# Kernel optimization log

Measured on AMD Instinct MI355X. Metric: run time of the kernel, lower is better.

## Reference

```python
import jax, jax.numpy as jnp
import numpy as np

S_DIM = 4096
N_NODES = 4096
N_EDGES = 32768


def _coarsen(ei_np, N):
    """Integer-only greedy coarsening, faithful to MNGRAPH.forward's while-loop.
    Returns (select order, flattened neighbor indices, segment ids, per-hub
    neighbor counts, forward-fill indices replicating the stale-M behavior for
    empty neighborhoods, and the remapped final edge_index)."""
    ei = ei_np.astype(np.int64).copy()
    I = np.bincount(ei[0], minlength=N)
    O = np.bincount(ei[1], minlength=N)
    order = np.argsort(-(I + O), kind='stable')  # torch.argsort(D, descending=True)
    visits = np.zeros(N, dtype=bool)
    select = []
    nbr_idx, nbr_seg, counts = [], [], []
    while order.size > 0:
        node = int(order[0])
        select.append(node)
        visits[node] = True
        # H = unique neighbors of node in the CURRENT (rewritten) edge_index
        H = np.unique(np.concatenate([ei[1][ei[0] == node], ei[0][ei[1] == node]]))
        visits[H] = True
        order = order[~visits[order]]
        # rewrite: endpoints in H that are not already-selected hubs -> node
        Hn = H[~np.isin(H, np.asarray(select, dtype=np.int64))]
        ei[np.isin(ei, Hn)] = node
        ei = ei[:, ei[0] != ei[1]]  # drop self-loops
        # append reversed edges that are not already present (pair-code isin
        # == the original O(E^2) all/any comparison, computed efficiently)
        code = ei[0] * N + ei[1]
        rcode = ei[1] * N + ei[0]
        new = ~np.isin(rcode, code)
        ei = np.concatenate([ei, ei[::-1][:, new]], axis=1)
        k = len(select) - 1
        nbr_idx.append(H)
        nbr_seg.append(np.full(H.shape[0], k, dtype=np.int64))
        counts.append(H.shape[0])
    select = np.asarray(select, dtype=np.int64)
    sort_sel = np.sort(select)
    ei_out = np.searchsorted(sort_sel, ei)  # compact node ids
    counts = np.asarray(counts, dtype=np.int64)
    # forward-fill: when H is empty the original appends the previous (stale) M
    fill = np.arange(select.shape[0])
    for i in range(select.shape[0]):
        if counts[i] == 0:
            fill[i] = fill[i - 1] if i > 0 else 0
    nbr = np.concatenate(nbr_idx) if nbr_idx else np.zeros(0, np.int64)
    seg = np.concatenate(nbr_seg) if nbr_seg else np.zeros(0, np.int64)
    return select, nbr, seg, counts, fill, ei_out


def setup_inputs() -> dict:
    key = jax.random.key(0)
    k1, k2, k3, k4 = jax.random.split(key, 4)
    x = jax.random.normal(k1, (N_NODES, S_DIM), dtype=jnp.float32)
    edge_index = jax.random.randint(k2, (2, N_EDGES), 0, N_NODES, dtype=jnp.int64)
    bound = float(np.sqrt(6.0 / (1.0 + S_DIM)))  # xavier_uniform on (1, S)
    W1 = jax.random.uniform(k3, (S_DIM,), jnp.float32, -bound, bound)
    W2 = jax.random.uniform(k4, (S_DIM,), jnp.float32, -bound, bound)
    B1 = jnp.zeros((S_DIM,), jnp.float32)
    B2 = jnp.zeros((S_DIM,), jnp.float32)
    return {"x": x, "edge_index": edge_index, "W1": W1, "W2": W2, "B1": B1, "B2": B2}


def reference(x, edge_index, W1, W2, B1, B2):
    N = x.shape[0]
    sel, nbr, seg, counts, fill, ei_out = _coarsen(np.asarray(edge_index), N)
    K = sel.shape[0]
    # Dn = x[n]*W1+B1 for every neighbor of every hub; per-hub mean via segment_sum
    Dn = x[jnp.asarray(nbr)] * W1 + B1                      # [T, S]
    sums = jax.ops.segment_sum(Dn, jnp.asarray(seg), num_segments=K)
    denom = jnp.maximum(jnp.asarray(counts), 1).astype(x.dtype)[:, None]
    mean_Dn = sums / denom                                  # [K, S]
    Dv = x[jnp.asarray(sel)] * W2 + B2                      # [K, S]
    END = jnp.concatenate([Dv, mean_Dn], axis=1)            # [K, 2S]
    END = END[jnp.asarray(fill)]                            # stale-M replication
    return END, jnp.asarray(ei_out)
```

## Files before the change

### kernel.cpp

```cpp
#include <hip/hip_runtime.h>
#include <hip/hip_bf16.h>

#define NT 1024
#define NNODES 4096
#define ECAP 65536

__global__ __launch_bounds__(256)
void zeroBM(int4* __restrict__ bm) {
    bm[(size_t)blockIdx.x * 256 + threadIdx.x] = make_int4(0, 0, 0, 0);
}

__device__ __forceinline__ int blockScanExcl(int v, int* s_w, int* total) {
    const int tid  = threadIdx.x;
    const int lane = tid & 63;
    const int wv   = tid >> 6;
    int x = v;
#pragma unroll
    for (int off = 1; off < 64; off <<= 1) {
        int t = __shfl_up(x, off, 64);
        if (lane >= off) x += t;
    }
    if (lane == 63) s_w[wv] = x;
    __syncthreads();
    if (tid < 16) {
        int y = s_w[tid];
#pragma unroll
        for (int off = 1; off < 16; off <<= 1) {
            int t = __shfl_up(y, off, 16);
            if (tid >= off) y += t;
        }
        s_w[tid] = y;
    }
    __syncthreads();
    int base = wv ? s_w[wv - 1] : 0;
    int tot  = s_w[15];
    __syncthreads();
    *total = tot;
    return base + x - v;
}

__global__ __launch_bounds__(NT, 1)
void phaseA1(const int* __restrict__ ei, int E0,
             int* __restrict__ U, int* __restrict__ V,
             unsigned int* __restrict__ BM,
             int* __restrict__ NBR, int* __restrict__ OTH,
             int* __restrict__ ORDV, int* __restrict__ ROFFG, int* __restrict__ RENDG,
             int* __restrict__ HAND)
{
    __shared__ unsigned short s_order[NNODES];
    __shared__ unsigned char  s_vis[NNODES];
    __shared__ unsigned char  s_rank[NNODES];
    __shared__ unsigned int   s_hb[NNODES / 32];
    __shared__ int s_roff[NNODES];
    __shared__ int s_rend[NNODES];
    __shared__ int s_tmp[NNODES];
    __shared__ int s_mat[64][65];
    __shared__ int s_w[16];
    __shared__ int s_bc[16];

    const int tid = threadIdx.x;

    for (int i = tid; i < NNODES; i += NT) { s_vis[i] = 0; s_tmp[i] = 0; }
    for (int i = tid; i < NNODES / 32; i += NT) s_hb[i] = 0;
    if (tid < 16) s_bc[tid] = 0;
    __syncthreads();

    for (int i = tid; i < E0; i += NT)
        if (ei[2 * i + 1] != 0) s_bc[9] = 1;
    __syncthreads();
    const int is64 = !s_bc[9];

    for (int e = tid; e < E0; e += NT) {
        int uu = ei[is64 ? 2 * e : e];
        int vv = ei[is64 ? 2 * (E0 + e) : (E0 + e)];
        U[e] = uu; V[e] = vv;
        atomicAdd(&s_tmp[uu], 1);
        atomicAdd(&s_tmp[vv], 1);
    }
    __syncthreads();
    for (int n = tid; n < NNODES; n += NT) atomicMax(&s_bc[7], s_tmp[n]);
    __syncthreads();
    const int maxd = s_bc[7];

    if (maxd < 64) {
        const int wv = tid >> 6, lane = tid & 63;
        const unsigned long long ltm = (1ull << lane) - 1ull;
        for (int g = wv; g < 64; g += 16) {
            int n = g * 64 + lane;
            int d = s_tmp[n];
            int rk = 0;
            for (int dd = 0; dd < 64; ++dd) {
                unsigned long long bal = __ballot(d == dd);
                if (lane == 0) s_mat[dd][g] = __popcll(bal);
                if (d == dd) rk = __popcll(bal & ltm);
            }
            s_rank[n] = (unsigned char)rk;
        }
        __syncthreads();
        if (tid < 64) {
            int run = 0;
            for (int g = 0; g < 64; ++g) { int t = s_mat[tid][g]; s_mat[tid][g] = run; run += t; }
            s_mat[tid][64] = run;
        }
        __syncthreads();
        if (tid < 64) {
            int x = s_mat[tid][64];
#pragma unroll
            for (int off = 1; off < 64; off <<= 1) {
                int t = __shfl_up(x, off, 64);
                if (tid >= off) x += t;
            }
            int T = __shfl(x, 63, 64);
            s_mat[tid][64] = T - x;
        }
        __syncthreads();
        for (int g = wv; g < 64; g += 16) {
            int n = g * 64 + lane;
            int d = s_tmp[n];
            int pos = s_mat[d][64] + s_mat[d][g] + (int)s_rank[n];
            s_order[pos] = (unsigned short)n;
        }
        __syncthreads();
    } else {
        for (int d = maxd; d >= 0; --d) {
            int n0 = tid * 4;
            int f0 = (s_tmp[n0] == d), f1 = (s_tmp[n0 + 1] == d);
            int f2 = (s_tmp[n0 + 2] == d), f3 = (s_tmp[n0 + 3] == d);
            int tot;
            int off = blockScanExcl(f0 + f1 + f2 + f3, s_w, &tot);
            int idx = s_bc[4] + off;
            if (f0) s_order[idx++] = (unsigned short)n0;
            if (f1) s_order[idx++] = (unsigned short)(n0 + 1);
            if (f2) s_order[idx++] = (unsigned short)(n0 + 2);
            if (f3) s_order[idx++] = (unsigned short)(n0 + 3);
            __syncthreads();
            if (tid == 0) s_bc[4] += tot;
            __syncthreads();
        }
    }

    if (tid == 0) {
        int nd = s_order[0];
        s_bc[0] = nd; s_vis[nd] = 1;
    }
    __syncthreads();
    {
        const int node = s_bc[0];
        for (int e = tid; e < E0; e += NT) {
            int uu = U[e], vv = V[e];
            if (uu == node) {
                int w = vv; unsigned m = 1u << (w & 31);
                unsigned old = atomicOr(&s_hb[w >> 5], m);
                if (!(old & m)) { int i = atomicAdd(&s_bc[2], 1); s_tmp[i] = w; s_vis[w] = 1; }
            }
            if (vv == node) {
                int w = uu; unsigned m = 1u << (w & 31);
                unsigned old = atomicOr(&s_hb[w >> 5], m);
                if (!(old & m)) { int i = atomicAdd(&s_bc[2], 1); s_tmp[i] = w; s_vis[w] = 1; }
            }
        }
        __syncthreads();
        for (int e = tid; e < E0; e += NT) {
            int uu = U[e];
            if (uu != node && ((s_hb[uu >> 5] >> (uu & 31)) & 1)) U[e] = node;
            int vv = V[e];
            if (vv != node && ((s_hb[vv >> 5] >> (vv & 31)) & 1)) V[e] = node;
        }
        __syncthreads();
    }

    for (int e = tid; e < E0; e += NT) {
        int uu = U[e], vv = V[e];
        if (uu != vv) {
            unsigned code = ((unsigned)uu << 12) | (unsigned)vv;
            atomicOr(&BM[code >> 5], 1u << (code & 31));
        }
    }
    __syncthreads();
    for (int t0 = 0; t0 < E0; t0 += NT * 32) {
        unsigned fm = 0u;
        const int base = t0 + tid * 32;
        for (int j = 0; j < 32; ++j) {
            int e = base + j;
            if (e < E0) {
                int uu = U[e], vv = V[e];
                if (uu != vv) {
                    unsigned rc = ((unsigned)vv << 12) | (unsigned)uu;
                    unsigned old = atomicOr(&BM[rc >> 5], 0u);
                    if (!((old >> (rc & 31)) & 1u)) fm |= (1u << j);
                }
            }
        }
        int tot;
        int off = blockScanExcl(__popc(fm), s_w, &tot);
        int r = s_bc[5] + off;
        unsigned m = fm;
        while (m) {
            int j = __ffs((int)m) - 1; m &= m - 1;
            int e = base + j;
            U[E0 + r] = V[e]; V[E0 + r] = U[e];
            ++r;
        }
        __syncthreads();
        if (tid == 0) s_bc[5] += tot;
        __syncthreads();
    }
    const int E1 = E0 + s_bc[5];

    for (int n = tid; n < NNODES; n += NT) s_roff[n] = 0;
    __syncthreads();
    for (int e = tid; e < E1; e += NT) {
        int uu = U[e], vv = V[e];
        if (uu != vv) atomicAdd(&s_roff[uu], 1);
    }
    __syncthreads();
    {
        int n0 = tid * 4;
        int c0 = s_roff[n0], c1 = s_roff[n0 + 1], c2 = s_roff[n0 + 2], c3 = s_roff[n0 + 3];
        int tot;
        int off = blockScanExcl(c0 + c1 + c2 + c3, s_w, &tot);
        int st = off;
        s_roff[n0] = st;     s_rend[n0] = st;     st += c0;
        s_roff[n0 + 1] = st; s_rend[n0 + 1] = st; st += c1;
        s_roff[n0 + 2] = st; s_rend[n0 + 2] = st; st += c2;
        s_roff[n0 + 3] = st; s_rend[n0 + 3] = st;
    }
    __syncthreads();
    for (int e = tid; e < E1; e += NT) {
        int uu = U[e], vv = V[e];
        if (uu != vv) {
            int p = atomicAdd(&s_rend[uu], 1);
            OTH[p] = vv;
        }
    }
    __syncthreads();
    {
        const int cnt0 = s_bc[2];
        for (int i = tid; i < cnt0; i += NT) NBR[i] = s_tmp[i];
    }
    for (int i = tid; i < NNODES; i += NT) {
        int nd = (int)s_order[i];
        ORDV[i]  = nd | (s_vis[nd] ? 0x8000 : 0);
        ROFFG[i] = s_roff[i];
        RENDG[i] = s_rend[i];
    }
    if (tid == 0) { HAND[0] = E1; HAND[1] = s_bc[2]; HAND[2] = s_bc[0]; }
}

__global__ __launch_bounds__(64, 1)
void phaseA2(const int* __restrict__ OTH, int* __restrict__ NBR,
             const int* __restrict__ ORDV, const int* __restrict__ ROFFG,
             const int* __restrict__ RENDG, const int* __restrict__ HAND,
             int* __restrict__ SEL, int* __restrict__ CNTS,
             int* __restrict__ NST, int* __restrict__ FIL, int* __restrict__ SC,
             int* __restrict__ LABG, int* __restrict__ RNKG)
{
    __shared__ unsigned short s_ordvis[NNODES];
    __shared__ unsigned short s_pos[NNODES];
    __shared__ unsigned short s_lab[NNODES];
    __shared__ unsigned short s_so[NNODES];
    __shared__ int s_cnt[NNODES];
    __shared__ int s_stamp[NNODES];
    __shared__ int s_roff[NNODES];
    __shared__ int s_rend[NNODES];
    __shared__ unsigned char s_sel[NNODES];

    const int ln = threadIdx.x;
    const unsigned long long ltm = (1ull << ln) - 1ull;
    const int cnt0 = HAND[1], hub0 = HAND[2];

    for (int i = ln; i < NNODES; i += 64) {
        int ov = ORDV[i];
        s_ordvis[i] = (unsigned short)ov;
        s_pos[ov & 0x7FFF] = (unsigned short)i;
        s_roff[i] = ROFFG[i];
        s_rend[i] = RENDG[i];
        s_lab[i] = (unsigned short)i;
        s_stamp[i] = 0; s_sel[i] = 0; s_cnt[i] = 0;
    }
    if (ln == 0) {
        s_sel[hub0] = 1; s_so[0] = (unsigned short)hub0;
        s_cnt[0] = cnt0;
    }

    int nc = cnt0;
    int p = 0, k = 1;
    int pf_node = -1, pf_rb = 0, pf_re = 0, pf_val = -1;

    for (;;) {
        int node = -1;
        while (p < NNODES) {
            int idx = p + ln;
            int ov = (idx < NNODES) ? (int)s_ordvis[idx] : 0x8000;
            unsigned long long bal = __ballot(!(ov & 0x8000));
            if (bal != 0ull) {
                int sl = __ffsll((long long)bal) - 1;
                node = __shfl(ov, sl, 64) & 0x7FFF;
                p += sl + 1;
                break;
            }
            p += 64;
        }
        if (node < 0) break;
        if (ln == 0) { s_sel[node] = 1; s_so[k] = (unsigned short)node; }

        int rb, re, v0;
        if (node == pf_node) { rb = pf_rb; re = pf_re; v0 = pf_val; }
        else {
            rb = s_roff[node]; re = s_rend[node];
            v0 = (rb + ln < re) ? OTH[rb + ln] : -1;
        }

        {
            int q = p, cand = -1, cidx = NNODES;
            while (q < NNODES) {
                int idx = q + ln;
                int ov = (idx < NNODES) ? (int)s_ordvis[idx] : 0x8000;
                unsigned long long bal = __ballot(!(ov & 0x8000));
                if (bal != 0ull) {
                    int sl = __ffsll((long long)bal) - 1;
                    cand = __shfl(ov, sl, 64) & 0x7FFF;
                    cidx = q + sl;
                    break;
                }
                q += 64;
            }
            p = (cand >= 0) ? cidx : NNODES;
            pf_node = cand;
            if (cand >= 0) {
                pf_rb = s_roff[cand]; pf_re = s_rend[cand];
                pf_val = (pf_rb + ln < pf_re) ? OTH[pf_rb + ln] : -1;
            } else pf_val = -1;
        }

        const int begin = nc;
        auto proc = [&](int o) {
            int w = (o >= 0) ? (int)s_lab[o] : node;
            bool cnd = (w != node);
            int old = k;
            if (cnd) old = atomicMax(&s_stamp[w], k);
            bool nw = cnd && (old < k);
            unsigned long long bal = __ballot(nw);
            if (nw) {
                int pre = __popcll(bal & ltm);
                NBR[nc + pre] = w;
                s_ordvis[s_pos[w]] = (unsigned short)(0x8000 | w);
                if (!s_sel[w]) s_lab[w] = (unsigned short)node;
            }
            nc += __popcll(bal);
        };
        proc(v0);
        for (int s0 = rb + 64; s0 < re; s0 += 64) {
            int o = (s0 + ln < re) ? OTH[s0 + ln] : -1;
            proc(o);
        }
        if (ln == 0) s_cnt[k] = nc - begin;
        k++;
    }
    const int K = k;

    {
        int base = 0;
        for (int c = 0; c < NNODES / 64; ++c) {
            int n = c * 64 + ln;
            int f = s_sel[n];
            unsigned long long b = __ballot(f);
            s_stamp[n] = base + __popcll(b & ltm);
            base += __popcll(b);
        }
    }
    {
        int nb = 0;
        for (int c = 0; c * 64 < K; ++c) {
            int i = c * 64 + ln;
            int cv = (i < K) ? s_cnt[i] : 0;
            int x = cv;
#pragma unroll
            for (int off = 1; off < 64; off <<= 1) {
                int t = __shfl_up(x, off, 64);
                if (ln >= off) x += t;
            }
            if (i < K) { NST[i] = nb + x - cv; CNTS[i] = cv; SEL[i] = (int)s_so[i]; }
            nb += __shfl(x, 63, 64);
        }
    }
    {
        int carry = 0;
        for (int c = 0; c * 64 < K; ++c) {
            int i = c * 64 + ln;
            int f = (i < K) && (s_cnt[i] > 0);
            unsigned long long b = __ballot(f);
            unsigned long long m = b & ((ln == 63) ? ~0ull : ((1ull << (ln + 1)) - 1ull));
            int fil = m ? (c * 64 + 63 - __clzll(m)) : carry;
            if (i < K) FIL[i] = fil;
            carry = b ? (c * 64 + 63 - __clzll(b)) : carry;
        }
    }
    if (ln == 0) SC[0] = K;
    for (int i = ln; i < NNODES; i += 64) {
        LABG[i] = (int)s_lab[i];
        RNKG[i] = s_stamp[i];
    }
}

__global__ __launch_bounds__(NT, 1)
void phaseA3(const int* __restrict__ U, const int* __restrict__ V,
             const int* __restrict__ LABG, const int* __restrict__ RNKG,
             const int* __restrict__ HAND, int* __restrict__ SC,
             int* __restrict__ TMP, float* __restrict__ out)
{
    __shared__ unsigned short l_lab[NNODES];
    __shared__ int l_rnk[NNODES];
    __shared__ int s_w[16];
    __shared__ int s_base[1];

    const int tid = threadIdx.x;
    for (int i = tid; i < NNODES; i += NT) {
        l_lab[i] = (unsigned short)LABG[i];
        l_rnk[i] = RNKG[i];
    }
    if (tid == 0) s_base[0] = 0;
    __syncthreads();

    const int E1 = HAND[0];
    const int K  = SC[0];
    const size_t obase = (size_t)K * 8192;

    for (int t0 = 0; t0 < E1; t0 += NT * 64) {
        unsigned long long fm = 0ull;
        const int base = t0 + tid * 64;
        if (base + 64 <= E1) {
            const int4* U4 = (const int4*)(U + base);
            const int4* V4 = (const int4*)(V + base);
#pragma unroll
            for (int q = 0; q < 16; ++q) {
                int4 a = U4[q], b = V4[q];
                int j = q * 4;
                if ((int)l_lab[a.x] != (int)l_lab[b.x]) fm |= 1ull << j;
                if ((int)l_lab[a.y] != (int)l_lab[b.y]) fm |= 1ull << (j + 1);
                if ((int)l_lab[a.z] != (int)l_lab[b.z]) fm |= 1ull << (j + 2);
                if ((int)l_lab[a.w] != (int)l_lab[b.w]) fm |= 1ull << (j + 3);
            }
        } else {
            for (int j = 0; j < 64; ++j) {
                int e = base + j;
                if (e < E1) {
                    if ((int)l_lab[U[e]] != (int)l_lab[V[e]]) fm |= 1ull << j;
                }
            }
        }
        int tot;
        int off = blockScanExcl(__popcll(fm), s_w, &tot);
        int r = s_base[0] + off;
        unsigned long long m = fm;
        while (m) {
            int j = __ffsll((long long)m) - 1; m &= m - 1;
            int e = base + j;
            out[obase + (size_t)r] = (float)l_rnk[(int)l_lab[U[e]]];
            TMP[r] = l_rnk[(int)l_lab[V[e]]];
            ++r;
        }
        __syncthreads();
        if (tid == 0) s_base[0] += tot;
        __syncthreads();
    }
    const int Ef = s_base[0];
    if (tid == 0) SC[1] = Ef;
    for (int r = tid; r < Ef; r += NT)
        out[obase + (size_t)Ef + (size_t)r] = (float)TMP[r];
}

__global__ __launch_bounds__(256, 4)
void phaseB(const float* __restrict__ x,
            const float* __restrict__ W1, const float* __restrict__ W2,
            const float* __restrict__ B1, const float* __restrict__ B2,
            const int* __restrict__ NBR, const int* __restrict__ SEL,
            const int* __restrict__ CNTS, const int* __restrict__ NST,
            const int* __restrict__ FIL, const int* __restrict__ SC,
            float* __restrict__ out)
{
    const int K = SC[0];
    const int k = blockIdx.x;
    if (k >= K) return;
    const int kk   = FIL[k];
    const int node = SEL[kk];
    const int cnt  = CNTS[kk];
    const int st   = NST[kk];
    const int tid  = threadIdx.x;
    const float4* x4 = (const float4*)x;

    float4 acc[4];
#pragma unroll
    for (int j = 0; j < 4; j++) acc[j] = make_float4(0.f, 0.f, 0.f, 0.f);

    for (int r = 0; r < cnt; ++r) {
        const float4* row = x4 + (size_t)NBR[st + r] * 1024;
#pragma unroll
        for (int j = 0; j < 4; j++) {
            float4 t = row[tid + j * 256];
            acc[j].x += t.x; acc[j].y += t.y; acc[j].z += t.z; acc[j].w += t.w;
        }
    }

    const float fc  = (float)cnt;
    const float inv = 1.0f / (float)(cnt > 1 ? cnt : 1);
    const float4* xr = x4 + (size_t)node * 1024;
    float4* o4 = (float4*)(out + (size_t)k * 8192);

#pragma unroll
    for (int j = 0; j < 4; j++) {
        int c = tid + j * 256;
        float4 w1 = ((const float4*)W1)[c], b1 = ((const float4*)B1)[c];
        float4 w2 = ((const float4*)W2)[c], b2 = ((const float4*)B2)[c];
        float4 xv = xr[c];
        float4 pd, pm;
        pd.x = xv.x * w2.x + b2.x;
        pd.y = xv.y * w2.y + b2.y;
        pd.z = xv.z * w2.z + b2.z;
        pd.w = xv.w * w2.w + b2.w;
        pm.x = (acc[j].x * w1.x + fc * b1.x) * inv;
        pm.y = (acc[j].y * w1.y + fc * b1.y) * inv;
        pm.z = (acc[j].z * w1.z + fc * b1.z) * inv;
        pm.w = (acc[j].w * w1.w + fc * b1.w) * inv;
        o4[c] = pd;
        o4[1024 + c] = pm;
    }
}

extern "C" void kernel_launch(void* const* d_in, const int* in_sizes, int n_in,
                              void* d_out, int out_size, void* d_ws, size_t ws_size,
                              hipStream_t stream)
{
    const float* x  = (const float*)d_in[0];
    const int*   ei = (const int*)d_in[1];
    const float* W1 = (const float*)d_in[2];
    const float* W2 = (const float*)d_in[3];
    const float* B1 = (const float*)d_in[4];
    const float* B2 = (const float*)d_in[5];
    const int E0 = in_sizes[1] / 2;

    char* w = (char*)d_ws;
    int* U = (int*)w;
    int* V = U + ECAP;
    unsigned int* BM = (unsigned int*)(V + ECAP);
    int* OTH = (int*)BM;
    int* NBR = OTH + 2 * ECAP;
    int* TMP = NBR + 2 * ECAP;
    char* meta = (char*)BM + (2u << 20);
    int* SEL   = (int*)meta;
    int* CNTS  = SEL  + NNODES;
    int* NST   = CNTS + NNODES;
    int* FIL   = NST  + NNODES;
    int* SC    = FIL  + NNODES;
    int* ORDV  = SC   + 16;
    int* ROFFG = ORDV + NNODES;
    int* RENDG = ROFFG + NNODES;
    int* LABG  = RENDG + NNODES;
    int* RNKG  = LABG + NNODES;
    int* HAND  = RNKG + NNODES;
    float* out = (float*)d_out;

    hipLaunchKernelGGL(zeroBM, dim3(512), dim3(256), 0, stream, (int4*)BM);

    hipLaunchKernelGGL(phaseA1, dim3(1), dim3(NT), 0, stream,
                       ei, E0, U, V, BM, NBR, OTH, ORDV, ROFFG, RENDG, HAND);
    hipLaunchKernelGGL(phaseA2, dim3(1), dim3(64), 0, stream,
                       OTH, NBR, ORDV, ROFFG, RENDG, HAND,
                       SEL, CNTS, NST, FIL, SC, LABG, RNKG);
    hipLaunchKernelGGL(phaseA3, dim3(1), dim3(NT), 0, stream,
                       U, V, LABG, RNKG, HAND, SC, TMP, out);
    hipLaunchKernelGGL(phaseB, dim3(NNODES), dim3(256), 0, stream,
                       x, W1, W2, B1, B2, NBR, SEL, CNTS, NST, FIL, SC, out);
}
```

Before: 1.190 ms.

## Replace ordered-visit scan with bitmask and speculatively select two hubs per step

The serial greedy hub-selection loop in phaseA2 now tracks visited order slots as a 4096-bit LDS bitmap instead of flag bits in a ushort array. The next unvisited hub is found with two ballots and find-first-set over 128 words rather than a linear 64-wide scan. Each iteration picks two candidate hubs at once and prefetches both adjacency rows. It re-selects the second hub if processing the first marks it visited. The aim is to shorten the serial critical path of one wavefront, at the cost of extra LDS atomics and more complex control flow.

Measured after the change: 1.061 ms. 10.9% less time.

```diff
diff --git a/kernel.cpp b/kernel.cpp
--- a/kernel.cpp
+++ b/kernel.cpp
@@ -255,7 +255,8 @@
              int* __restrict__ NST, int* __restrict__ FIL, int* __restrict__ SC,
              int* __restrict__ LABG, int* __restrict__ RNKG)
 {
-    __shared__ unsigned short s_ordvis[NNODES];
+    __shared__ unsigned short s_ord[NNODES];
+    __shared__ unsigned int   s_visbits[NNODES / 32];
     __shared__ unsigned short s_pos[NNODES];
     __shared__ unsigned short s_lab[NNODES];
     __shared__ unsigned short s_so[NNODES];
@@ -269,14 +270,17 @@
     const unsigned long long ltm = (1ull << ln) - 1ull;
     const int cnt0 = HAND[1], hub0 = HAND[2];
 
+    for (int i = ln; i < NNODES / 32; i += 64) s_visbits[i] = 0u;
     for (int i = ln; i < NNODES; i += 64) {
         int ov = ORDV[i];
-        s_ordvis[i] = (unsigned short)ov;
-        s_pos[ov & 0x7FFF] = (unsigned short)i;
+        int nd = ov & 0x7FFF;
+        s_ord[i] = (unsigned short)nd;
+        s_pos[nd] = (unsigned short)i;
         s_roff[i] = ROFFG[i];
         s_rend[i] = RENDG[i];
         s_lab[i] = (unsigned short)i;
         s_stamp[i] = 0; s_sel[i] = 0; s_cnt[i] = 0;
+        if (ov & 0x8000) atomicOr(&s_visbits[i >> 5], 1u << (i & 31));
     }
     if (ln == 0) {
         s_sel[hub0] = 1; s_so[0] = (unsigned short)hub0;
@@ -284,59 +288,76 @@
     }
 
     int nc = cnt0;
-    int p = 0, k = 1;
-    int pf_node = -1, pf_rb = 0, pf_re = 0, pf_val = -1;
-
-    for (;;) {
-        int node = -1;
-        while (p < NNODES) {
-            int idx = p + ln;
-            int ov = (idx < NNODES) ? (int)s_ordvis[idx] : 0x8000;
-            unsigned long long bal = __ballot(!(ov & 0x8000));
-            if (bal != 0ull) {
-                int sl = __ffsll((long long)bal) - 1;
-                node = __shfl(ov, sl, 64) & 0x7FFF;
-                p += sl + 1;
-                break;
-            }
-            p += 64;
-        }
-        if (node < 0) break;
-        if (ln == 0) { s_sel[node] = 1; s_so[k] = (unsigned short)node; }
-
-        int rb, re, v0;
-        if (node == pf_node) { rb = pf_rb; re = pf_re; v0 = pf_val; }
-        else {
-            rb = s_roff[node]; re = s_rend[node];
-            v0 = (rb + ln < re) ? OTH[rb + ln] : -1;
-        }
-
-        {
-            int q = p, cand = -1, cidx = NNODES;
-            while (q < NNODES) {
-                int idx = q + ln;
-                int ov = (idx < NNODES) ? (int)s_ordvis[idx] : 0x8000;
-                unsigned long long bal = __ballot(!(ov & 0x8000));
-                if (bal != 0ull) {
-                    int sl = __ffsll((long long)bal) - 1;
-                    cand = __shfl(ov, sl, 64) & 0x7FFF;
-                    cidx = q + sl;
-                    break;
+    int k = 1;
+
+    auto select2 = [&](int& c1, int& c2) {
+        unsigned lo = ~s_visbits[ln];
+        unsigned hi = ~s_visbits[ln + 64];
+        unsigned long long ball = __ballot(lo != 0u);
+        unsigned long long balh = __ballot(hi != 0u);
+        c1 = -1; c2 = -1;
+        int slot2 = -1;
+        if (ball) {
+            int sl = __ffsll((long long)ball) - 1;
+            unsigned ww = __shfl(lo, sl, 64);
+            int slot1 = sl * 32 + __ffs((int)ww) - 1;
+            c1 = (int)s_ord[slot1];
+            unsigned wwb = ww & (ww - 1);
+            if (wwb) slot2 = sl * 32 + __ffs((int)wwb) - 1;
+            else {
+                unsigned long long ball2 = ball & (ball - 1);
+                if (ball2) {
+                    int sl2 = __ffsll((long long)ball2) - 1;
+                    unsigned ww2 = __shfl(lo, sl2, 64);
+                    slot2 = sl2 * 32 + __ffs((int)ww2) - 1;
+                } else if (balh) {
+                    int sl2 = __ffsll((long long)balh) - 1;
+                    unsigned ww2 = __shfl(hi, sl2, 64);
+                    slot2 = 2048 + sl2 * 32 + __ffs((int)ww2) - 1;
                 }
-                q += 64;
-            }
-            p = (cand >= 0) ? cidx : NNODES;
-            pf_node = cand;
-            if (cand >= 0) {
-                pf_rb = s_roff[cand]; pf_re = s_rend[cand];
-                pf_val = (pf_rb + ln < pf_re) ? OTH[pf_rb + ln] : -1;
-            } else pf_val = -1;
-        }
-
-        const int begin = nc;
-        auto proc = [&](int o) {
-            int w = (o >= 0) ? (int)s_lab[o] : node;
-            bool cnd = (w != node);
+            }
+        } else if (balh) {
+            int sl = __ffsll((long long)balh) - 1;
+            unsigned ww = __shfl(hi, sl, 64);
+            int slot1 = 2048 + sl * 32 + __ffs((int)ww) - 1;
+            c1 = (int)s_ord[slot1];
+            unsigned wwb = ww & (ww - 1);
+            if (wwb) slot2 = 2048 + sl * 32 + __ffs((int)wwb) - 1;
+            else {
+                unsigned long long balh2 = balh & (balh - 1);
+                if (balh2) {
+                    int sl2 = __ffsll((long long)balh2) - 1;
+                    unsigned ww2 = __shfl(hi, sl2, 64);
+                    slot2 = 2048 + sl2 * 32 + __ffs((int)ww2) - 1;
+                }
+            }
+        }
+        if (slot2 >= 0) c2 = (int)s_ord[slot2];
+    };
+
+    auto select1 = [&](int& c) {
+        unsigned lo = ~s_visbits[ln];
+        unsigned hi = ~s_visbits[ln + 64];
+        unsigned long long ball = __ballot(lo != 0u);
+        unsigned long long balh = __ballot(hi != 0u);
+        c = -1;
+        if (ball) {
+            int sl = __ffsll((long long)ball) - 1;
+            unsigned ww = __shfl(lo, sl, 64);
+            c = (int)s_ord[sl * 32 + __ffs((int)ww) - 1];
+        } else if (balh) {
+            int sl = __ffsll((long long)balh) - 1;
+            unsigned ww = __shfl(hi, sl, 64);
+            c = (int)s_ord[2048 + sl * 32 + __ffs((int)ww) - 1];
+        }
+    };
+
+    auto procRow = [&](int hub, int rb, int re, int o0, int watch) -> bool {
+        bool invw = false;
+        int o = o0;
+        for (int s0 = rb; s0 < re; s0 += 64) {
+            int w = (o >= 0) ? (int)s_lab[o] : hub;
+            bool cnd = (w != hub);
             int old = k;
             if (cnd) old = atomicMax(&s_stamp[w], k);
             bool nw = cnd && (old < k);
@@ -344,16 +365,59 @@
             if (nw) {
                 int pre = __popcll(bal & ltm);
                 NBR[nc + pre] = w;
-                s_ordvis[s_pos[w]] = (unsigned short)(0x8000 | w);
-                if (!s_sel[w]) s_lab[w] = (unsigned short)node;
+                int slot = (int)s_pos[w];
+                atomicOr(&s_visbits[slot >> 5], 1u << (slot & 31));
+                if (!s_sel[w]) s_lab[w] = (unsigned short)hub;
             }
             nc += __popcll(bal);
-        };
-        proc(v0);
-        for (int s0 = rb + 64; s0 < re; s0 += 64) {
-            int o = (s0 + ln < re) ? OTH[s0 + ln] : -1;
-            proc(o);
-        }
+            invw = invw || (__ballot(nw && (w == watch)) != 0ull);
+            int s1 = s0 + 64;
+            o = (s1 + ln < re) ? OTH[s1 + ln] : -1;
+        }
+        return invw;
+    };
+
+    for (;;) {
+        int c1, c2;
+        select2(c1, c2);
+        if (c1 < 0) break;
+
+        int rb1 = s_roff[c1], re1 = s_rend[c1];
+        int rb2 = (c2 >= 0) ? s_roff[c2] : 0;
+        int re2 = (c2 >= 0) ? s_rend[c2] : 0;
+        int oA = (rb1 + ln < re1) ? OTH[rb1 + ln] : -1;
+        int oB = (c2 >= 0 && rb2 + ln < re2) ? OTH[rb2 + ln] : -1;
+
+        if (ln == 0) {
+            s_sel[c1] = 1; s_so[k] = (unsigned short)c1;
+            int sl1 = (int)s_pos[c1];
+            atomicOr(&s_visbits[sl1 >> 5], 1u << (sl1 & 31));
+            if (c2 >= 0) {
+                int sl2 = (int)s_pos[c2];
+                atomicOr(&s_visbits[sl2 >> 5], 1u << (sl2 & 31));
+            }
+        }
+
+        int begin = nc;
+        bool inval = procRow(c1, rb1, re1, oA, c2);
+        if (ln == 0) s_cnt[k] = nc - begin;
+        k++;
+
+        if (c2 < 0) continue;
+
+        if (inval) {
+            select1(c2);
+            if (c2 < 0) continue;
+            rb2 = s_roff[c2]; re2 = s_rend[c2];
+            oB = (rb2 + ln < re2) ? OTH[rb2 + ln] : -1;
+        }
+        if (ln == 0) {
+            s_sel[c2] = 1; s_so[k] = (unsigned short)c2;
+            int sl2 = (int)s_pos[c2];
+            atomicOr(&s_visbits[sl2 >> 5], 1u << (sl2 & 31));
+        }
+        begin = nc;
+        procRow(c2, rb2, re2, oB, -1);
         if (ln == 0) s_cnt[k] = nc - begin;
         k++;
     }
```

## Use visited bitmask and batch four hub candidates per iteration in greedy coarsening

Applied to the files above, without the earlier changes.

Replaces the per-slot visited ordering array with a 4096-bit visited bitmap held in shared memory, scanned by wave ballots. Each outer iteration extracts up to four next unvisited candidates and issues their first adjacency loads together, cancelling later candidates if an earlier hub's row visits them. Label, position and selected flags are packed into one 32-bit metadata word, which cuts shared-memory lookups per neighbor. The aim is to shorten the serial single-wave critical path. The cost is extra ballots to detect candidate conflicts and more complex control flow.

New measurement: 1.047 ms. 1.14x faster.

```diff
diff --git a/kernel.cpp b/kernel.cpp
--- a/kernel.cpp
+++ b/kernel.cpp
@@ -255,107 +255,166 @@
              int* __restrict__ NST, int* __restrict__ FIL, int* __restrict__ SC,
              int* __restrict__ LABG, int* __restrict__ RNKG)
 {
-    __shared__ unsigned short s_ordvis[NNODES];
-    __shared__ unsigned short s_pos[NNODES];
-    __shared__ unsigned short s_lab[NNODES];
+    __shared__ unsigned short s_ord[NNODES];
+    __shared__ unsigned int   s_visbits[NNODES / 32];
+    __shared__ unsigned int   s_meta[NNODES];
     __shared__ unsigned short s_so[NNODES];
     __shared__ int s_cnt[NNODES];
     __shared__ int s_stamp[NNODES];
     __shared__ int s_roff[NNODES];
     __shared__ int s_rend[NNODES];
-    __shared__ unsigned char s_sel[NNODES];
 
     const int ln = threadIdx.x;
     const unsigned long long ltm = (1ull << ln) - 1ull;
     const int cnt0 = HAND[1], hub0 = HAND[2];
 
+    for (int i = ln; i < NNODES / 32; i += 64) s_visbits[i] = 0u;
     for (int i = ln; i < NNODES; i += 64) {
         int ov = ORDV[i];
-        s_ordvis[i] = (unsigned short)ov;
-        s_pos[ov & 0x7FFF] = (unsigned short)i;
+        int nd = ov & 0x7FFF;
+        s_ord[i] = (unsigned short)nd;
+        s_meta[nd] = ((unsigned)i << 16) | (unsigned)nd;
         s_roff[i] = ROFFG[i];
         s_rend[i] = RENDG[i];
-        s_lab[i] = (unsigned short)i;
-        s_stamp[i] = 0; s_sel[i] = 0; s_cnt[i] = 0;
+        s_stamp[i] = 0; s_cnt[i] = 0;
+        if (ov & 0x8000) atomicOr(&s_visbits[i >> 5], 1u << (i & 31));
     }
     if (ln == 0) {
-        s_sel[hub0] = 1; s_so[0] = (unsigned short)hub0;
+        s_meta[hub0] = (unsigned)hub0 | 0x8000u;
+        s_so[0] = (unsigned short)hub0;
         s_cnt[0] = cnt0;
     }
 
     int nc = cnt0;
-    int p = 0, k = 1;
-    int pf_node = -1, pf_rb = 0, pf_re = 0, pf_val = -1;
-
-    for (;;) {
-        int node = -1;
-        while (p < NNODES) {
-            int idx = p + ln;
-            int ov = (idx < NNODES) ? (int)s_ordvis[idx] : 0x8000;
-            unsigned long long bal = __ballot(!(ov & 0x8000));
-            if (bal != 0ull) {
-                int sl = __ffsll((long long)bal) - 1;
-                node = __shfl(ov, sl, 64) & 0x7FFF;
-                p += sl + 1;
-                break;
-            }
-            p += 64;
-        }
-        if (node < 0) break;
-        if (ln == 0) { s_sel[node] = 1; s_so[k] = (unsigned short)node; }
-
-        int rb, re, v0;
-        if (node == pf_node) { rb = pf_rb; re = pf_re; v0 = pf_val; }
-        else {
-            rb = s_roff[node]; re = s_rend[node];
-            v0 = (rb + ln < re) ? OTH[rb + ln] : -1;
-        }
-
-        {
-            int q = p, cand = -1, cidx = NNODES;
-            while (q < NNODES) {
-                int idx = q + ln;
-                int ov = (idx < NNODES) ? (int)s_ordvis[idx] : 0x8000;
-                unsigned long long bal = __ballot(!(ov & 0x8000));
-                if (bal != 0ull) {
-                    int sl = __ffsll((long long)bal) - 1;
-                    cand = __shfl(ov, sl, 64) & 0x7FFF;
-                    cidx = q + sl;
-                    break;
-                }
-                q += 64;
-            }
-            p = (cand >= 0) ? cidx : NNODES;
-            pf_node = cand;
-            if (cand >= 0) {
-                pf_rb = s_roff[cand]; pf_re = s_rend[cand];
-                pf_val = (pf_rb + ln < pf_re) ? OTH[pf_rb + ln] : -1;
-            } else pf_val = -1;
-        }
-
-        const int begin = nc;
-        auto proc = [&](int o) {
-            int w = (o >= 0) ? (int)s_lab[o] : node;
-            bool cnd = (w != node);
+    int k = 1;
+
+    unsigned lo = 0u, hi = 0u;
+    auto reload = [&]() { lo = ~s_visbits[ln]; hi = ~s_visbits[ln + 64]; };
+    auto extract = [&]() -> int {
+        unsigned long long b = __ballot(lo != 0u);
+        if (b) {
+            int sl = __ffsll((long long)b) - 1;
+            unsigned ww = __shfl(lo, sl, 64);
+            if (ln == sl) lo &= lo - 1;
+            return sl * 32 + (__ffs((int)ww) - 1);
+        }
+        b = __ballot(hi != 0u);
+        if (b) {
+            int sl = __ffsll((long long)b) - 1;
+            unsigned ww = __shfl(hi, sl, 64);
+            if (ln == sl) hi &= hi - 1;
+            return 2048 + sl * 32 + (__ffs((int)ww) - 1);
+        }
+        return -1;
+    };
+
+    auto procRow = [&](int hub, int hslot, int rb, int re, int o0,
+                       int wA, int wB, int wC) -> int {
+        const unsigned relv = ((unsigned)hslot << 16) | (unsigned)hub | 0x8000u;
+        const bool haveW = (wA >= 0) | (wB >= 0) | (wC >= 0);
+        int hitm = 0;
+        int o = o0;
+        for (int s0 = rb; s0 < re; s0 += 64) {
+            unsigned g = (o >= 0) ? s_meta[o] : 0u;
+            int w = (o >= 0) ? (int)(g & 0x7FFFu) : hub;
+            bool cnd = (w != hub);
             int old = k;
             if (cnd) old = atomicMax(&s_stamp[w], k);
             bool nw = cnd && (old < k);
             unsigned long long bal = __ballot(nw);
             if (nw) {
-                int pre = __popcll(bal & ltm);
-                NBR[nc + pre] = w;
-                s_ordvis[s_pos[w]] = (unsigned short)(0x8000 | w);
-                if (!s_sel[w]) s_lab[w] = (unsigned short)node;
+                NBR[nc + __popcll(bal & ltm)] = w;
+                int slot = (int)(g >> 16);
+                atomicOr(&s_visbits[slot >> 5], 1u << (slot & 31));
+                if (!(g & 0x8000u)) s_meta[w] = relv;
             }
             nc += __popcll(bal);
-        };
-        proc(v0);
-        for (int s0 = rb + 64; s0 < re; s0 += 64) {
-            int o = (s0 + ln < re) ? OTH[s0 + ln] : -1;
-            proc(o);
-        }
+            if (haveW) {
+                bool aw = nw && (w == wA || w == wB || w == wC);
+                if (__ballot(aw) != 0ull) {
+                    if (__ballot(nw && w == wA)) hitm |= 1;
+                    if (__ballot(nw && w == wB)) hitm |= 2;
+                    if (__ballot(nw && w == wC)) hitm |= 4;
+                }
+            }
+            int s1 = s0 + 64;
+            o = (s1 + ln < re) ? OTH[s1 + ln] : -1;
+        }
+        return hitm;
+    };
+
+    for (;;) {
+        reload();
+        int sl0 = extract();
+        if (sl0 < 0) break;
+        int sl1 = extract(), sl2 = -1, sl3 = -1;
+        if (sl1 >= 0) { sl2 = extract(); if (sl2 >= 0) sl3 = extract(); }
+
+        int c0 = (int)s_ord[sl0];
+        int c1 = (sl1 >= 0) ? (int)s_ord[sl1] : -1;
+        int c2 = (sl2 >= 0) ? (int)s_ord[sl2] : -1;
+        int c3 = (sl3 >= 0) ? (int)s_ord[sl3] : -1;
+
+        {
+            int ms = (ln == 0) ? sl0 : (ln == 1) ? sl1 : (ln == 2) ? sl2 : sl3;
+            if (ln < 4 && ms >= 0) atomicOr(&s_visbits[ms >> 5], 1u << (ms & 31));
+        }
+
+        int rb0 = s_roff[c0], re0 = s_rend[c0];
+        int rb1 = 0, re1 = 0, rb2 = 0, re2 = 0, rb3 = 0, re3 = 0;
+        if (c1 >= 0) { rb1 = s_roff[c1]; re1 = s_rend[c1]; }
+        if (c2 >= 0) { rb2 = s_roff[c2]; re2 = s_rend[c2]; }
+        if (c3 >= 0) { rb3 = s_roff[c3]; re3 = s_rend[c3]; }
+        int v0 = (rb0 + ln < re0) ? OTH[rb0 + ln] : -1;
+        int v1 = (c1 >= 0 && rb1 + ln < re1) ? OTH[rb1 + ln] : -1;
+        int v2 = (c2 >= 0 && rb2 + ln < re2) ? OTH[rb2 + ln] : -1;
+        int v3 = (c3 >= 0 && rb3 + ln < re3) ? OTH[rb3 + ln] : -1;
+
+        if (ln == 0) {
+            s_meta[c0] = ((unsigned)sl0 << 16) | (unsigned)c0 | 0x8000u;
+            s_so[k] = (unsigned short)c0;
+        }
+        int begin = nc;
+        int hit = procRow(c0, sl0, rb0, re0, v0, c1, c2, c3);
         if (ln == 0) s_cnt[k] = nc - begin;
         k++;
+        if (hit & 1) c1 = -1;
+        if (hit & 2) c2 = -1;
+        if (hit & 4) c3 = -1;
+
+        if (c1 >= 0) {
+            if (ln == 0) {
+                s_meta[c1] = ((unsigned)sl1 << 16) | (unsigned)c1 | 0x8000u;
+                s_so[k] = (unsigned short)c1;
+            }
+            begin = nc;
+            hit = procRow(c1, sl1, rb1, re1, v1, c2, c3, -1);
+            if (ln == 0) s_cnt[k] = nc - begin;
+            k++;
+            if (hit & 1) c2 = -1;
+            if (hit & 2) c3 = -1;
+        }
+        if (c2 >= 0) {
+            if (ln == 0) {
+                s_meta[c2] = ((unsigned)sl2 << 16) | (unsigned)c2 | 0x8000u;
+                s_so[k] = (unsigned short)c2;
+            }
+            begin = nc;
+            hit = procRow(c2, sl2, rb2, re2, v2, c3, -1, -1);
+            if (ln == 0) s_cnt[k] = nc - begin;
+            k++;
+            if (hit & 1) c3 = -1;
+        }
+        if (c3 >= 0) {
+            if (ln == 0) {
+                s_meta[c3] = ((unsigned)sl3 << 16) | (unsigned)c3 | 0x8000u;
+                s_so[k] = (unsigned short)c3;
+            }
+            begin = nc;
+            procRow(c3, sl3, rb3, re3, v3, -1, -1, -1);
+            if (ln == 0) s_cnt[k] = nc - begin;
+            k++;
+        }
     }
     const int K = k;
 
@@ -363,7 +422,8 @@
         int base = 0;
         for (int c = 0; c < NNODES / 64; ++c) {
             int n = c * 64 + ln;
-            int f = s_sel[n];
+            unsigned mv = s_meta[n];
+            int f = ((mv & 0x8000u) != 0u) && ((int)(mv & 0x7FFFu) == n);
             unsigned long long b = __ballot(f);
             s_stamp[n] = base + __popcll(b & ltm);
             base += __popcll(b);
@@ -398,7 +458,7 @@
     }
     if (ln == 0) SC[0] = K;
     for (int i = ln; i < NNODES; i += 64) {
-        LABG[i] = (int)s_lab[i];
+        LABG[i] = (int)(s_meta[i] & 0x7FFFu);
         RNKG[i] = s_stamp[i];
     }
 }
```
